# Kernel optimization log

Hardware: AMD Instinct MI355X
Metric: run time of the kernel (lower is better)

The kernel has to match this reference:

```python
import jax, jax.numpy as jnp
import numpy as np
import math

N_HEAD = 32
ROPE_BASE = 10000.0


def _rope_headwise(x):
    # Faithful to the source bug: x is [B, H, S, D] and the rotary module uses
    # x.shape[1] (= H) as the "sequence length", so the angle depends on the
    # head index, broadcast over the true sequence axis.
    B, H, S, D = x.shape
    inv_freq = 1.0 / (ROPE_BASE ** (jnp.arange(0, D, 2, dtype=jnp.float32) / D))  # [D/2]
    t = jnp.arange(H, dtype=jnp.float32)                                          # [H]
    freqs = t[:, None] * inv_freq[None, :]                                        # [H, D/2]
    # emb = cat(freqs, freqs)[..., :D//2] == freqs, so cos/sin are just over freqs
    cos = jnp.cos(freqs)[None, :, None, :]   # [1, H, 1, D/2]
    sin = jnp.sin(freqs)[None, :, None, :]
    x1, x2 = x[..., : D // 2], x[..., D // 2 :]
    return jnp.concatenate([x1 * cos - x2 * sin, x1 * sin + x2 * cos], axis=-1)


def setup_inputs() -> dict:
    key = jax.random.key(0)
    ks = jax.random.split(key, 5)
    B, S, E = 2, 2048, 2048
    scale = 0.02
    return {
        "x": jax.random.normal(ks[0], (B, S, E), dtype=jnp.float32),
        "Wq": jax.random.normal(ks[1], (E, E), dtype=jnp.float32) * scale,
        "bq": jnp.zeros((E,), dtype=jnp.float32),
        "Wk": jax.random.normal(ks[2], (E, E), dtype=jnp.float32) * scale,
        "bk": jnp.zeros((E,), dtype=jnp.float32),
        "Wv": jax.random.normal(ks[3], (E, E), dtype=jnp.float32) * scale,
        "bv": jnp.zeros((E,), dtype=jnp.float32),
        "Wo": jax.random.normal(ks[4], (E, E), dtype=jnp.float32) * scale,
        "bo": jnp.zeros((E,), dtype=jnp.float32),
    }


def reference(x, Wq, bq, Wk, bk, Wv, bv, Wo, bo):
    B, S, E = x.shape
    H = N_HEAD
    D = E // H

    def split_heads(y):  # [B,S,E] -> [B,H,S,D]
        return y.reshape(B, S, H, D).transpose(0, 2, 1, 3)

    q = split_heads(x @ Wq + bq)
    k = split_heads(x @ Wk + bk)
    v = split_heads(x @ Wv + bv)

    q = _rope_headwise(q)
    k = _rope_headwise(k)

    scores = jnp.einsum("bhqd,bhkd->bhqk", q, k) / math.sqrt(D)  # [B,H,S,S]
    causal = jnp.triu(jnp.ones((S, S), dtype=bool), k=1)
    scores = jnp.where(causal[None, None], -jnp.inf, scores)
    attn = jax.nn.softmax(scores, axis=-1)
    out = jnp.einsum("bhqk,bhkd->bhqd", attn, v)                 # [B,H,S,D]
    out = out.transpose(0, 2, 1, 3).reshape(B, S, E)
    return out @ Wo + bo
```

## Files before the change

### kernel.cpp

```cpp
#include <hip/hip_runtime.h>
#include <hip/hip_bf16.h>

#define B_ 2
#define S_ 2048
#define E_ 2048
#define H_ 32
#define M_ (B_*S_)

typedef __bf16 bf16x8 __attribute__((ext_vector_type(8)));
typedef float  f32x4  __attribute__((ext_vector_type(4)));

__device__ __forceinline__ ushort f2bf(float f) {
    uint u = __float_as_uint(f);
    u += 0x7fffu + ((u >> 16) & 1u);
    return (ushort)(u >> 16);
}
__device__ __forceinline__ uint pack2bf(float a, float b) {
    __hip_bfloat162 h = __float22bfloat162_rn(make_float2(a, b));
    return *(uint*)&h;
}
__device__ __forceinline__ float bf2f(ushort h) {
    return __uint_as_float(((uint)h) << 16);
}
__device__ __forceinline__ f32x4 f4zero() {
    f32x4 z; z[0]=0.f; z[1]=0.f; z[2]=0.f; z[3]=0.f; return z;
}
__device__ __forceinline__ void async16(const ushort* g, ushort* l) {
    __builtin_amdgcn_global_load_lds((const __attribute__((address_space(1))) void*)g,
                                     (__attribute__((address_space(3))) void*)l, 16, 0, 0);
}

__global__ __launch_bounds__(256) void cast_x_kernel(const float* __restrict__ x,
                                                     ushort* __restrict__ xb) {
    int i = (blockIdx.x * 256 + threadIdx.x) * 4;
    float4 v = *(const float4*)(x + i);
    uint2 o;
    o.x = pack2bf(v.x, v.y);
    o.y = pack2bf(v.z, v.w);
    *(uint2*)(xb + i) = o;
}

__global__ __launch_bounds__(256) void wtrans_kernel(const float* __restrict__ W0, const float* __restrict__ W1,
                                                     const float* __restrict__ W2, const float* __restrict__ W3,
                                                     ushort* __restrict__ T0, ushort* __restrict__ T1,
                                                     ushort* __restrict__ T2, ushort* __restrict__ T3) {
    const float* W = (blockIdx.z==0)?W0:(blockIdx.z==1)?W1:(blockIdx.z==2)?W2:W3;
    ushort*      T = (blockIdx.z==0)?T0:(blockIdx.z==1)?T1:(blockIdx.z==2)?T2:T3;
    __shared__ float tile[64][65];
    const int k0 = blockIdx.y * 64, n0 = blockIdx.x * 64;
    const int rr = threadIdx.x >> 4;
    const int cc = (threadIdx.x & 15) * 4;
    #pragma unroll
    for (int p = 0; p < 4; ++p) {
        int r = p * 16 + rr;
        float4 v = *(const float4*)(W + (size_t)(k0 + r) * E_ + n0 + cc);
        tile[r][cc+0] = v.x; tile[r][cc+1] = v.y; tile[r][cc+2] = v.z; tile[r][cc+3] = v.w;
    }
    __syncthreads();
    #pragma unroll
    for (int p = 0; p < 4; ++p) {
        int rn = p * 16 + rr;
        uint2 o;
        o.x = pack2bf(tile[cc+0][rn], tile[cc+1][rn]);
        o.y = pack2bf(tile[cc+2][rn], tile[cc+3][rn]);
        *(uint2*)(T + (size_t)(n0 + rn) * E_ + k0 + cc) = o;
    }
}

__global__ __launch_bounds__(256) void vtrans_kernel(const ushort* __restrict__ vb,
                                                     ushort* __restrict__ vt) {
    __shared__ ushort tile[64][65];
    const int bh = blockIdx.y, b = bh >> 5, h = bh & 31;
    const int s0 = blockIdx.x * 64;
    int tx = threadIdx.x & 63, ty = threadIdx.x >> 6;
    #pragma unroll
    for (int it = 0; it < 16; ++it) {
        int r = it * 4 + ty;
        tile[r][tx] = vb[(size_t)(b * S_ + s0 + r) * E_ + h * 64 + tx];
    }
    __syncthreads();
    #pragma unroll
    for (int it = 0; it < 16; ++it) {
        int r = it * 4 + ty;
        vt[(size_t)(bh * 64 + r) * S_ + s0 + tx] = tile[tx][r];
    }
}

template<bool OUTF32, bool DOROPE, int NZ>
__global__ __launch_bounds__(256) void gemm128(const ushort* __restrict__ A,
        const ushort* __restrict__ Bt0, const ushort* __restrict__ Bt1, const ushort* __restrict__ Bt2,
        const float* __restrict__ bias0, const float* __restrict__ bias1, const float* __restrict__ bias2,
        void* __restrict__ C0, void* __restrict__ C1, void* __restrict__ C2) {
    const int bid = blockIdx.x;
    const int z   = bid % NZ;
    const int nb  = (bid / NZ) % (E_ / 128);
    const int mb  = bid / (NZ * (E_ / 128));

    const ushort* Bt  = (z==0)?Bt0:(z==1)?Bt1:Bt2;
    const float* bias = (z==0)?bias0:(z==1)?bias1:bias2;
    void* Cv          = (z==0)?C0:(z==1)?C1:C2;

    __shared__ ushort As[128 * 64];
    __shared__ ushort Bs[128 * 64];

    const int tid  = threadIdx.x;
    const int wave = tid >> 6, lane = tid & 63;
    const int quad = lane >> 4, l15 = lane & 15;
    const int wm = wave >> 1, wn = wave & 1;
    const int m0 = mb * 128, n0 = nb * 128;
    const int srow = tid >> 3;
    const int scgx = (tid & 7) ^ (srow & 7);

    f32x4 acc[4][4];
    #pragma unroll
    for (int i = 0; i < 4; ++i)
        #pragma unroll
        for (int j = 0; j < 4; ++j) acc[i][j] = f4zero();

    for (int k0 = 0; k0 < E_; k0 += 64) {
        #pragma unroll
        for (int it = 0; it < 4; ++it) {
            int r = it * 32 + srow;
            async16(A  + (size_t)(m0 + r) * E_ + k0 + scgx * 8, As + (it * 256 + wave * 64) * 8);
            async16(Bt + (size_t)(n0 + r) * E_ + k0 + scgx * 8, Bs + (it * 256 + wave * 64) * 8);
        }
        __syncthreads();
        #pragma unroll
        for (int kk = 0; kk < 2; ++kk) {
            bf16x8 af[4], bfr[4];
            #pragma unroll
            for (int mt = 0; mt < 4; ++mt) {
                int row = wm * 64 + mt * 16 + l15;
                af[mt] = *(const bf16x8*)(As + row * 64 + (((kk * 4 + quad) ^ (row & 7)) << 3));
            }
            #pragma unroll
            for (int nt = 0; nt < 4; ++nt) {
                int row = wn * 64 + nt * 16 + l15;
                bfr[nt] = *(const bf16x8*)(Bs + row * 64 + (((kk * 4 + quad) ^ (row & 7)) << 3));
            }
            #pragma unroll
            for (int mt = 0; mt < 4; ++mt)
                #pragma unroll
                for (int nt = 0; nt < 4; ++nt)
                    acc[mt][nt] = __builtin_amdgcn_mfma_f32_16x16x32_bf16(af[mt], bfr[nt], acc[mt][nt], 0, 0, 0);
        }
        __syncthreads();
    }

    if (DOROPE && z != 2) {
        const float qsc = (z == 0) ? 0.125f * 1.44269504f : 1.0f;
        const int h = (n0 + wn * 64) >> 6;
        float sn[2], cs[2];
        #pragma unroll
        for (int nt = 0; nt < 2; ++nt) {
            int j = nt * 16 + l15;
            float ang = (float)h * __expf(-(float)j * 0.28782313662425575f);
            __sincosf(ang, &sn[nt], &cs[nt]);
        }
        ushort* C = (ushort*)Cv;
        #pragma unroll
        for (int mt = 0; mt < 4; ++mt) {
            #pragma unroll
            for (int nt = 0; nt < 2; ++nt) {
                int col1 = n0 + wn * 64 + nt * 16 + l15;
                float b1 = bias[col1], b2 = bias[col1 + 32];
                #pragma unroll
                for (int r = 0; r < 4; ++r) {
                    int rowg = m0 + wm * 64 + mt * 16 + quad * 4 + r;
                    float x1 = acc[mt][nt][r] + b1;
                    float x2 = acc[mt][nt + 2][r] + b2;
                    C[(size_t)rowg * E_ + col1]      = f2bf((x1 * cs[nt] - x2 * sn[nt]) * qsc);
                    C[(size_t)rowg * E_ + col1 + 32] = f2bf((x1 * sn[nt] + x2 * cs[nt]) * qsc);
                }
            }
        }
    } else {
        #pragma unroll
        for (int mt = 0; mt < 4; ++mt) {
            #pragma unroll
            for (int nt = 0; nt < 4; ++nt) {
                int col = n0 + wn * 64 + nt * 16 + l15;
                float bv = bias[col];
                #pragma unroll
                for (int r = 0; r < 4; ++r) {
                    int rowg = m0 + wm * 64 + mt * 16 + quad * 4 + r;
                    float v = acc[mt][nt][r] + bv;
                    if (OUTF32) ((float*)Cv)[(size_t)rowg * E_ + col] = v;
                    else        ((ushort*)Cv)[(size_t)rowg * E_ + col] = f2bf(v);
                }
            }
        }
    }
}

__global__ __launch_bounds__(256) void flash_kernel(const ushort* __restrict__ qb,
        const ushort* __restrict__ kb, const ushort* __restrict__ vt,
        ushort* __restrict__ ctx) {
    __shared__ ushort KVs[2][2][64 * 64];
    __shared__ ushort Ps[4][32 * 64];

    const int tid  = threadIdx.x;
    const int wave = tid >> 6, lane = tid & 63;
    const int quad = lane >> 4, l15 = lane & 15;
    const int bh = blockIdx.y, b = bh >> 5, h = bh & 31;
    const int srow = tid >> 3;
    const int scgx = (tid & 7) ^ (srow & 7);
    ushort* Pw = Ps[wave];

    bf16x8 ones;
    #pragma unroll
    for (int j = 0; j < 8; ++j) ones[j] = (__bf16)1.0f;

    #pragma unroll 1
    for (int pass = 0; pass < 2; ++pass) {
        const int qx  = pass ? (15 - (int)blockIdx.x) : (int)blockIdx.x;
        const int q0  = qx * 128;
        const int qw0 = q0 + wave * 32;
        const int nkt = 2 * qx + 2;

        bf16x8 qf[2][2];
        #pragma unroll
        for (int mt = 0; mt < 2; ++mt)
            #pragma unroll
            for (int kk = 0; kk < 2; ++kk)
                qf[mt][kk] = *(const bf16x8*)(qb + (size_t)(b * S_ + qw0 + mt * 16 + l15) * E_ + h * 64 + kk * 32 + quad * 8);

        f32x4 oacc[2][4], lacc[2];
        #pragma unroll
        for (int mt = 0; mt < 2; ++mt) {
            lacc[mt] = f4zero();
            #pragma unroll
            for (int dt = 0; dt < 4; ++dt) oacc[mt][dt] = f4zero();
        }

        #pragma unroll
        for (int it = 0; it < 2; ++it) {
            int r = it * 32 + srow;
            async16(kb + (size_t)(b * S_ + r) * E_ + h * 64 + scgx * 8, KVs[0][0] + (it * 256 + wave * 64) * 8);
            async16(vt + (size_t)(bh * 64 + r) * S_ + scgx * 8,         KVs[0][1] + (it * 256 + wave * 64) * 8);
        }
        __syncthreads();

        #pragma unroll 1
        for (int kt = 0; kt < nkt; ++kt) {
            const int k0 = kt * 64;
            if (kt + 1 < nkt) {
                const int kn = k0 + 64;
                ushort* Kd = KVs[(kt + 1) & 1][0];
                ushort* Vd = KVs[(kt + 1) & 1][1];
                #pragma unroll
                for (int it = 0; it < 2; ++it) {
                    int r = it * 32 + srow;
                    async16(kb + (size_t)(b * S_ + kn + r) * E_ + h * 64 + scgx * 8, Kd + (it * 256 + wave * 64) * 8);
                    async16(vt + (size_t)(bh * 64 + r) * S_ + kn + scgx * 8,         Vd + (it * 256 + wave * 64) * 8);
                }
            }

            if (k0 <= qw0 + 31) {
                const ushort* Ks = KVs[kt & 1][0];
                const ushort* Vs = KVs[kt & 1][1];
                f32x4 sacc[2][4];
                #pragma unroll
                for (int mt = 0; mt < 2; ++mt)
                    #pragma unroll
                    for (int nt = 0; nt < 4; ++nt) sacc[mt][nt] = f4zero();
                #pragma unroll
                for (int kk = 0; kk < 2; ++kk)
                    #pragma unroll
                    for (int nt = 0; nt < 4; ++nt) {
                        int row = nt * 16 + l15;
                        bf16x8 kf = *(const bf16x8*)(Ks + row * 64 + (((kk * 4 + quad) ^ (row & 7)) << 3));
                        #pragma unroll
                        for (int mt = 0; mt < 2; ++mt)
                            sacc[mt][nt] = __builtin_amdgcn_mfma_f32_16x16x32_bf16(kf, qf[mt][kk], sacc[mt][nt], 0, 0, 0);
                    }

                #pragma unroll
                for (int mt = 0; mt < 2; ++mt) {
                    const int q  = qw0 + mt * 16 + l15;
                    const bool dm = (k0 + 63 > qw0 + mt * 16);
                    const int ql = mt * 16 + l15, swz = ql & 7;
                    #pragma unroll
                    for (int nt = 0; nt < 4; ++nt) {
                        float p[4];
                        #pragma unroll
                        for (int r = 0; r < 4; ++r) {
                            int s = k0 + nt * 16 + quad * 4 + r;
                            p[r] = exp2f(sacc[mt][nt][r]);
                            if (dm && s > q) p[r] = 0.f;
                        }
                        uint2 pk;
                        pk.x = pack2bf(p[0], p[1]);
                        pk.y = pack2bf(p[2], p[3]);
                        *(uint2*)(Pw + ql * 64 + (((nt * 2 + (quad >> 1)) ^ swz) << 3) + (quad & 1) * 4) = pk;
                    }
                }

                #pragma unroll
                for (int kk = 0; kk < 2; ++kk) {
                    bf16x8 pf[2];
                    #pragma unroll
                    for (int mt = 0; mt < 2; ++mt) {
                        int ql = mt * 16 + l15;
                        pf[mt] = *(const bf16x8*)(Pw + ql * 64 + (((kk * 4 + quad) ^ (ql & 7)) << 3));
                    }
                    #pragma unroll
                    for (int mt = 0; mt < 2; ++mt)
                        lacc[mt] = __builtin_amdgcn_mfma_f32_16x16x32_bf16(pf[mt], ones, lacc[mt], 0, 0, 0);
                    #pragma unroll
                    for (int dt = 0; dt < 4; ++dt) {
                        int row = dt * 16 + l15;
                        bf16x8 vf = *(const bf16x8*)(Vs + row * 64 + (((kk * 4 + quad) ^ (row & 7)) << 3));
                        #pragma unroll
                        for (int mt = 0; mt < 2; ++mt)
                            oacc[mt][dt] = __builtin_amdgcn_mfma_f32_16x16x32_bf16(pf[mt], vf, oacc[mt][dt], 0, 0, 0);
                    }
                }
            }
            __syncthreads();
        }

        #pragma unroll
        for (int mt = 0; mt < 2; ++mt)
            #pragma unroll
            for (int r = 0; r < 4; ++r) {
                float inv = 1.0f / lacc[mt][r];
                #pragma unroll
                for (int dt = 0; dt < 4; ++dt)
                    ctx[(size_t)(b * S_ + qw0 + mt * 16 + quad * 4 + r) * E_ + h * 64 + dt * 16 + l15] =
                        f2bf(oacc[mt][dt][r] * inv);
            }
    }
}

extern "C" void kernel_launch(void* const* d_in, const int* in_sizes, int n_in,
                              void* d_out, int out_size, void* d_ws, size_t ws_size,
                              hipStream_t stream) {
    const float* x  = (const float*)d_in[0];
    const float* Wq = (const float*)d_in[1];
    const float* bq = (const float*)d_in[2];
    const float* Wk = (const float*)d_in[3];
    const float* bk = (const float*)d_in[4];
    const float* Wv = (const float*)d_in[5];
    const float* bv = (const float*)d_in[6];
    const float* Wo = (const float*)d_in[7];
    const float* bo = (const float*)d_in[8];
    float* out = (float*)d_out;

    ushort* p   = (ushort*)d_ws;
    ushort* xb  = p; p += (size_t)M_ * E_;
    ushort* wqt = p; p += (size_t)E_ * E_;
    ushort* wkt = p; p += (size_t)E_ * E_;
    ushort* wvt = p; p += (size_t)E_ * E_;
    ushort* wot = p; p += (size_t)E_ * E_;
    ushort* qb  = p; p += (size_t)M_ * E_;
    ushort* kb  = p; p += (size_t)M_ * E_;
    ushort* vb  = p; p += (size_t)M_ * E_;
    ushort* ctx = p; p += (size_t)M_ * E_;
    ushort* vt  = xb;

    cast_x_kernel<<<(M_ * E_) / 1024, 256, 0, stream>>>(x, xb);
    wtrans_kernel<<<dim3(E_ / 64, E_ / 64, 4), 256, 0, stream>>>(Wq, Wk, Wv, Wo, wqt, wkt, wvt, wot);
    gemm128<false, true, 3><<<(E_ / 128) * (M_ / 128) * 3, 256, 0, stream>>>(
        xb, wqt, wkt, wvt, bq, bk, bv, qb, kb, vb);
    vtrans_kernel<<<dim3(S_ / 64, B_ * H_), 256, 0, stream>>>(vb, vt);
    flash_kernel<<<dim3(8, B_ * H_), 256, 0, stream>>>(qb, kb, vt, ctx);
    gemm128<true, false, 1><<<(E_ / 128) * (M_ / 128), 256, 0, stream>>>(
        ctx, wot, wot, wot, bo, bo, bo, out, out, out);
}
```

Measured before the change: 407.2 us.

## Replace QKV projection GEMM with 256x256-tile 8-wave double-buffered pipelined kernel

Adds a gemm256 kernel that computes 256x256 output tiles with 512 threads. It double-buffers LDS, splits each tile's K-step into four quarter-phases, and interleaves async global-to-LDS loads with MFMA work using explicit waitcnt, barrier and setprio control. The fused QKV projection now uses it in place of the 128x128 gemm128, aiming for more data reuse per tile and better overlap of loads with compute. The cost is much higher LDS and register use per block and fewer blocks in the grid (384), which may limit occupancy or leave CUs idle. The hand-tuned waitcnt ordering is fragile to get right.

```diff
diff --git a/kernel.cpp b/kernel.cpp
--- a/kernel.cpp
+++ b/kernel.cpp
@@ -85,6 +85,152 @@
         vt[(size_t)(bh * 64 + r) * S_ + s0 + tx] = tile[tx][r];
     }
 }
+
+#define VMW4 asm volatile("s_waitcnt vmcnt(4)" ::: "memory")
+#define VMW0 asm volatile("s_waitcnt vmcnt(0)" ::: "memory")
+#define MEMB asm volatile("" ::: "memory")
+
+#define STA_(bf, kt, h) { _Pragma("unroll") for (int it_ = 0; it_ < 2; ++it_) { \
+    async16(A + (size_t)(m0 + it_*128 + (h)*64 + srow) * E_ + (kt)*64 + scg*8,  \
+            &As[bf][(it_*128 + (h)*64 + wave*8) * 64]); } }
+
+#define STB_(bf, kt, h) { _Pragma("unroll") for (int it_ = 0; it_ < 2; ++it_) { \
+    int rih_ = it_*64 + srow;                                                   \
+    int ldr_ = ((rih_ >> 5) << 6) + (h)*32 + (rih_ & 31);                       \
+    int rwb_ = it_*64 + wave*8;                                                 \
+    int wbs_ = ((rwb_ >> 5) << 6) + (h)*32 + (rwb_ & 31);                       \
+    async16(Bt + (size_t)(n0 + ldr_) * E_ + (kt)*64 + scg*8,                    \
+            &Bs[bf][wbs_ * 64]); } }
+
+#define PHASE_(bf, mh, nh, STAGES) {                                            \
+    bf16x8 paf[4][2], pbf[2][2];                                                \
+    _Pragma("unroll") for (int m_ = 0; m_ < 4; ++m_)                            \
+      _Pragma("unroll") for (int k_ = 0; k_ < 2; ++k_) {                        \
+        int row_ = wm*128 + ((mh)*4 + m_)*16 + l15;                             \
+        paf[m_][k_] = *(const bf16x8*)(&As[bf][row_*64 + (((k_*4 + quad) ^ (row_ & 7)) << 3)]); } \
+    _Pragma("unroll") for (int n_ = 0; n_ < 2; ++n_)                            \
+      _Pragma("unroll") for (int k_ = 0; k_ < 2; ++k_) {                        \
+        int row_ = wn*64 + ((nh)*2 + n_)*16 + l15;                              \
+        pbf[n_][k_] = *(const bf16x8*)(&Bs[bf][row_*64 + (((k_*4 + quad) ^ (row_ & 7)) << 3)]); } \
+    STAGES;                                                                     \
+    MEMB; __builtin_amdgcn_s_barrier();                                         \
+    asm volatile("s_waitcnt lgkmcnt(0)" ::: "memory");                          \
+    __builtin_amdgcn_sched_barrier(0);                                          \
+    __builtin_amdgcn_s_setprio(1);                                              \
+    _Pragma("unroll") for (int k_ = 0; k_ < 2; ++k_)                            \
+      _Pragma("unroll") for (int m_ = 0; m_ < 4; ++m_)                          \
+        _Pragma("unroll") for (int n_ = 0; n_ < 2; ++n_)                        \
+          acc[(mh)*4+m_][(nh)*2+n_] = __builtin_amdgcn_mfma_f32_16x16x32_bf16(  \
+              paf[m_][k_], pbf[n_][k_], acc[(mh)*4+m_][(nh)*2+n_], 0, 0, 0);    \
+    __builtin_amdgcn_s_setprio(0);                                              \
+    MEMB; __builtin_amdgcn_s_barrier(); MEMB;                                   \
+  }
+
+template<bool OUTF32, bool DOROPE, int NZ>
+__global__ __launch_bounds__(512, 2) void gemm256(const ushort* __restrict__ A,
+        const ushort* __restrict__ Bt0, const ushort* __restrict__ Bt1, const ushort* __restrict__ Bt2,
+        const float* __restrict__ bias0, const float* __restrict__ bias1, const float* __restrict__ bias2,
+        void* __restrict__ C0, void* __restrict__ C1, void* __restrict__ C2) {
+    const int bid = blockIdx.x;
+    const int z   = bid % NZ;
+    const int nb  = (bid / NZ) % (E_ / 256);
+    const int mb  = bid / (NZ * (E_ / 256));
+
+    const ushort* Bt  = (z==0)?Bt0:(z==1)?Bt1:Bt2;
+    const float* bias = (z==0)?bias0:(z==1)?bias1:bias2;
+    void* Cv          = (z==0)?C0:(z==1)?C1:C2;
+
+    __shared__ ushort As[2][256 * 64];
+    __shared__ ushort Bs[2][256 * 64];
+
+    const int tid  = threadIdx.x;
+    const int wave = tid >> 6, lane = tid & 63;
+    const int quad = lane >> 4, l15 = lane & 15;
+    const int wm = wave >> 2, wn = wave & 3;
+    const int m0 = mb * 256, n0 = nb * 256;
+    const int srow = tid >> 3;
+    const int scg  = (tid & 7) ^ (srow & 7);
+
+    f32x4 acc[8][4];
+    #pragma unroll
+    for (int i = 0; i < 8; ++i)
+        #pragma unroll
+        for (int j = 0; j < 4; ++j) acc[i][j] = f4zero();
+
+    STB_(0, 0, 1); STA_(0, 0, 1); STA_(0, 0, 0); STB_(0, 0, 0);
+    STB_(1, 1, 1); STA_(1, 1, 1);
+    VMW4;
+    MEMB; __builtin_amdgcn_s_barrier(); MEMB;
+
+    #pragma unroll 1
+    for (int i = 0; i < 15; ++i) {
+        const int t1 = 2*i + 1, t2 = 2*i + 2, t3 = 2*i + 3;
+        PHASE_(0, 0, 1, STA_(1, t1, 0));
+        PHASE_(0, 1, 1, STB_(1, t1, 0));
+        PHASE_(0, 1, 0, STB_(0, t2, 1));
+        PHASE_(0, 0, 0, STA_(0, t2, 1); VMW4);
+        PHASE_(1, 0, 1, STA_(0, t2, 0));
+        PHASE_(1, 1, 1, STB_(0, t2, 0));
+        PHASE_(1, 1, 0, STB_(1, t3, 1));
+        PHASE_(1, 0, 0, STA_(1, t3, 1); VMW4);
+    }
+    PHASE_(0, 0, 1, STA_(1, 31, 0));
+    PHASE_(0, 1, 1, STB_(1, 31, 0));
+    PHASE_(0, 1, 0, {});
+    PHASE_(0, 0, 0, VMW0);
+    PHASE_(1, 0, 1, {});
+    PHASE_(1, 1, 1, {});
+    PHASE_(1, 1, 0, {});
+    PHASE_(1, 0, 0, {});
+
+    if (DOROPE && z != 2) {
+        const float qsc = (z == 0) ? 0.125f * 1.44269504f : 1.0f;
+        const int h = (n0 + wn * 64) >> 6;
+        float sn[2], cs[2];
+        #pragma unroll
+        for (int nt = 0; nt < 2; ++nt) {
+            int j = nt * 16 + l15;
+            float ang = (float)h * __expf(-(float)j * 0.28782313662425575f);
+            __sincosf(ang, &sn[nt], &cs[nt]);
+        }
+        ushort* C = (ushort*)Cv;
+        #pragma unroll
+        for (int f = 0; f < 8; ++f) {
+            #pragma unroll
+            for (int nt = 0; nt < 2; ++nt) {
+                int col1 = n0 + wn * 64 + nt * 16 + l15;
+                float b1 = bias[col1], b2 = bias[col1 + 32];
+                #pragma unroll
+                for (int r = 0; r < 4; ++r) {
+                    int rowg = m0 + wm * 128 + f * 16 + quad * 4 + r;
+                    float x1 = acc[f][nt][r] + b1;
+                    float x2 = acc[f][nt + 2][r] + b2;
+                    C[(size_t)rowg * E_ + col1]      = f2bf((x1 * cs[nt] - x2 * sn[nt]) * qsc);
+                    C[(size_t)rowg * E_ + col1 + 32] = f2bf((x1 * sn[nt] + x2 * cs[nt]) * qsc);
+                }
+            }
+        }
+    } else {
+        #pragma unroll
+        for (int f = 0; f < 8; ++f) {
+            #pragma unroll
+            for (int nt = 0; nt < 4; ++nt) {
+                int col = n0 + wn * 64 + nt * 16 + l15;
+                float bv = bias[col];
+                #pragma unroll
+                for (int r = 0; r < 4; ++r) {
+                    int rowg = m0 + wm * 128 + f * 16 + quad * 4 + r;
+                    float v = acc[f][nt][r] + bv;
+                    if (OUTF32) ((float*)Cv)[(size_t)rowg * E_ + col] = v;
+                    else        ((ushort*)Cv)[(size_t)rowg * E_ + col] = f2bf(v);
+                }
+            }
+        }
+    }
+}
+#undef STA_
+#undef STB_
+#undef PHASE_
 
 template<bool OUTF32, bool DOROPE, int NZ>
 __global__ __launch_bounds__(256) void gemm128(const ushort* __restrict__ A,
@@ -361,7 +507,7 @@
 
     cast_x_kernel<<<(M_ * E_) / 1024, 256, 0, stream>>>(x, xb);
     wtrans_kernel<<<dim3(E_ / 64, E_ / 64, 4), 256, 0, stream>>>(Wq, Wk, Wv, Wo, wqt, wkt, wvt, wot);
-    gemm128<false, true, 3><<<(E_ / 128) * (M_ / 128) * 3, 256, 0, stream>>>(
+    gemm256<false, true, 3><<<(E_ / 256) * (M_ / 256) * 3, 512, 0, stream>>>(
         xb, wqt, wkt, wvt, bq, bk, bv, qb, kb, vb);
     vtrans_kernel<<<dim3(S_ / 64, B_ * H_), 256, 0, stream>>>(vb, vt);
     flash_kernel<<<dim3(8, B_ * H_), 256, 0, stream>>>(qb, kb, vt, ctx);
```

Result: slower. 443.6 us (+8.9%).
